# Optimization experiments

Hardware: AMD Instinct MI355X
Metric: run time of the kernel (lower is better)

Reference implementation:

```python
import jax, jax.numpy as jnp
import numpy as np

B, NPG, DEG = 256, 256, 8        # graphs, nodes/graph, avg degree
IN_C, HID, OUT_C = 64, 64, 64
N = B * NPG                      # 65536 nodes
E = N * DEG                      # 524288 edges
K = NPG // 2                     # ASAP ratio=0.5 -> 128 kept nodes per graph


def setup_inputs() -> dict:
    key = jax.random.key(0)
    ks = jax.random.split(key, 12)
    x = jax.random.normal(ks[0], (N, IN_C), jnp.float32)
    # within-graph random edges, no self loops (ASAP adds remaining self loops itself)
    g = jnp.arange(E) // (NPG * DEG)
    src_l = jax.random.randint(ks[1], (E,), 0, NPG)
    off = jax.random.randint(ks[2], (E,), 1, NPG)
    dst_l = (src_l + off) % NPG
    edge_index = jnp.stack([src_l + g * NPG, dst_l + g * NPG]).astype(jnp.int32)
    batch = (jnp.arange(N) // NPG).astype(jnp.int32)
    def lin(k, fi, fo):
        return jax.random.normal(k, (fi, fo), jnp.float32) / np.sqrt(fi)
    return {
        "x": x, "edge_index": edge_index, "batch": batch,
        "W1": lin(ks[3], IN_C, HID), "b1": jnp.zeros((HID,), jnp.float32),
        "lin_W": lin(ks[4], HID, HID), "lin_b": jnp.zeros((HID,), jnp.float32),
        "att_W": lin(ks[5], 2 * HID, 1), "att_b": jnp.zeros((1,), jnp.float32),
        "le1_W": lin(ks[6], HID, 1), "le1_b": jnp.zeros((1,), jnp.float32),
        "le2_W": lin(ks[7], HID, 1),
        "le3_W": lin(ks[8], HID, 1), "le3_b": jnp.zeros((1,), jnp.float32),
        "W2": lin(ks[9], HID, OUT_C), "b2": jnp.zeros((OUT_C,), jnp.float32),
    }


def reference(x, edge_index, batch, W1, b1, lin_W, lin_b, att_W, att_b,
              le1_W, le1_b, le2_W, le3_W, le3_b, W2, b2):
    src, dst = edge_index[0], edge_index[1]
    dt = x.dtype

    # ---- conv1: GCNConv(in, hid) with self loops + symmetric norm ----
    h = x @ W1
    deg = jnp.zeros((N,), dt).at[dst].add(1.0) + 1.0  # +1 self loop
    dinv = jax.lax.rsqrt(deg)
    coef = dinv[src] * dinv[dst]
    h1 = jax.ops.segment_sum(h[src] * coef[:, None], dst, N) \
         + h * (dinv * dinv)[:, None] + b1
    h1 = jax.nn.relu(h1)  # dropout is identity at inference

    # ---- ASAPooling(hid, ratio=0.5): add remaining self loops ----
    sl = jnp.arange(N)
    srcF = jnp.concatenate([src, sl])
    dstF = jnp.concatenate([dst, sl])

    x_pool_j = h1[srcF]                                   # [Ef, HID]
    x_q = jax.ops.segment_max(x_pool_j, dstF, N)          # master-node max
    x_q = (x_q @ lin_W + lin_b)[dstF]
    s = (jnp.concatenate([x_q, x_pool_j], axis=-1) @ att_W + att_b)[:, 0]
    s = jax.nn.leaky_relu(s, 0.2)
    # segment softmax over edges grouped by target
    smax = jax.ops.segment_max(s, dstF, N)
    e = jnp.exp(s - smax[dstF])
    score = e / (jax.ops.segment_sum(e, dstF, N) + 1e-16)[dstF]
    xnew = jax.ops.segment_sum(h1[srcF] * score[:, None], dstF, N)

    # fitness = sigmoid(LEConv(xnew, edges_with_self_loops))
    # LEConv: out_i = sum_{j->i}(lin1(x_j) - lin2(x_i)) + lin3(x_i)
    a = xnew @ le1_W + le1_b
    b2_ = xnew @ le2_W
    degF = jnp.zeros((N,), dt).at[dstF].add(1.0)
    fit = jax.ops.segment_sum(a[srcF], dstF, N)[:, 0] - degF * b2_[:, 0] \
          + (xnew @ le3_W + le3_b)[:, 0]
    fitness = jax.nn.sigmoid(fit)

    # top-k (ratio=0.5) per graph; equal contiguous graphs -> static shapes
    _, topi = jax.lax.top_k(fitness.reshape(B, NPG), K)   # [B, K]
    perm = (topi + jnp.arange(B)[:, None] * NPG).reshape(-1)
    x_sel = xnew[perm] * fitness[perm][:, None]           # [B*K, HID]

    # graph coarsening: A' = S^T A S (dense per graph), diag removed
    g_e = dstF // NPG
    sL = srcF - g_e * NPG
    dL = dstF - g_e * NPG
    A = jnp.zeros((B, NPG, NPG), dt).at[g_e, sL, dL].add(1.0)
    S = jnp.zeros((B, NPG, NPG), dt).at[g_e, sL, dL].add(score)
    Ssel = jnp.take_along_axis(S, topi[:, None, :], axis=2)   # [B, NPG, K]
    AS = jnp.einsum('bij,bjk->bik', A, Ssel)                  # A @ S
    A2 = jnp.einsum('bji,bjk->bik', Ssel, AS)                 # S^T (A S) -> [B,K,K]
    A2 = A2 * (1.0 - jnp.eye(K, dtype=dt))                    # remove_diag

    # ---- conv2: GCNConv(hid, out); returned edge_weight is discarded in
    # the original forward, so edges are binary (nnz of A') + self loops ----
    M = (A2 > 0).astype(dt) + jnp.eye(K, dtype=dt)            # [B, src, dst]
    h2 = (x_sel @ W2).reshape(B, K, OUT_C)
    deg2 = M.sum(axis=1)                                      # in-degree per target
    d2 = jax.lax.rsqrt(deg2)
    Mn = M * d2[:, :, None] * d2[:, None, :]
    out2 = jnp.einsum('bsd,bsf->bdf', Mn, h2) + b2            # [B, K, OUT_C]

    # ---- global_mean_pool over each graph's K kept nodes ----
    return out2.mean(axis=1)                                  # [B, OUT_C]
```

## Files before the change

kernel.cpp:

```cpp
#include <hip/hip_runtime.h>

typedef float f4 __attribute__((ext_vector_type(4)));
typedef unsigned long long u64;

#define NPGL 256
#define EPGL 2048
#define HIDD 64
#define KKEEP 128
#define NTH 1024

__device__ __forceinline__ int swz(int n, int c) {
  return (n << 6) + ((((c ^ n) ^ (n >> 4)) & 15) << 2);
}

__global__ void __launch_bounds__(NTH)
asap_fused(const float* __restrict__ x, const int* __restrict__ ei,
           const float* __restrict__ W1, const float* __restrict__ b1,
           const float* __restrict__ linW, const float* __restrict__ linb,
           const float* __restrict__ attW, const float* __restrict__ attb,
           const float* __restrict__ le1W, const float* __restrict__ le1b,
           const float* __restrict__ le2W,
           const float* __restrict__ le3W, const float* __restrict__ le3b,
           const float* __restrict__ W2, const float* __restrict__ b2,
           float* __restrict__ out, int Etot)
{
  const int g = blockIdx.x;
  const int tid = threadIdx.x;

  __shared__ __align__(16) float buf[NPGL * HIDD];
  __shared__ __align__(16) float mskf[4096];
  __shared__ __align__(16) float esc[EPGL];
  __shared__ __align__(8) unsigned char csrc[4096];
  __shared__ unsigned short rowstU[NPGL + 1];
  __shared__ unsigned short rowstP[NPGL + 1];
  __shared__ int cnt[NPGL];
  __shared__ float dinv_[NPGL];
  __shared__ float sA[NPGL], sB[NPGL];
  __shared__ float rsf[NPGL];
  __shared__ float u_[HIDD], wsum[HIDD];
  __shared__ int scanw[4], scanwP[4];
  __shared__ float c0s;

  u64* Imask = (u64*)mskf;
  u64* Rmask = ((u64*)mskf) + 1024;
  u64* conn  = ((u64*)mskf) + 1536;
  int*   kept = (int*)(mskf + 3584);
  float* d2A  = mskf + 3712;
  float* cA   = mskf + 3840;

  const int ebase = g * EPGL;
  const int nbase = g * NPGL;

  ((u64*)mskf)[tid] = 0ull;
  if (tid < NPGL) { cnt[tid] = 0; ((u64*)mskf)[1536 + tid] = 0ull; }
  __syncthreads();

  int es[2], ed[2];
#pragma unroll
  for (int i = 0; i < 2; ++i) {
    const int e = tid + i * NTH;
    es[i] = ei[ebase + e] - nbase;
    ed[i] = ei[Etot + ebase + e] - nbase;
    atomicAdd(&cnt[ed[i]], 1);
  }
  {
    const f4* xg = (const f4*)(x + (size_t)nbase * HIDD);
#pragma unroll
    for (int ii = 0; ii < 4; ++ii) {
      const int i = tid + ii * NTH;
      *(f4*)&buf[swz(i >> 4, i & 15)] = xg[i];
    }
  }
  __syncthreads();

  int sU = 0, sP = 0, mU = 0;
  if (tid < NPGL) {
    mU = cnt[tid];
    const int mP = (mU + 7) & ~7;
    sU = mU; sP = mP;
#pragma unroll
    for (int off = 1; off < 64; off <<= 1) {
      const int uU = __shfl_up(sU, off, 64);
      const int uP = __shfl_up(sP, off, 64);
      if ((tid & 63) >= off) { sU += uU; sP += uP; }
    }
    if ((tid & 63) == 63) { scanw[tid >> 6] = sU; scanwP[tid >> 6] = sP; }
  }
  __syncthreads();
  if (tid < NPGL) {
    int aU = 0, aP = 0;
    const int w = tid >> 6;
    for (int ww = 0; ww < w; ++ww) { aU += scanw[ww]; aP += scanwP[ww]; }
    rowstU[tid + 1] = (unsigned short)(sU + aU);
    rowstP[tid + 1] = (unsigned short)(sP + aP);
    if (tid == 0) { rowstU[0] = 0; rowstP[0] = 0; }
    cnt[tid] = 0;
    dinv_[tid] = rsqrtf((float)mU + 1.0f);
  }
  if (tid < HIDD) {
    float a = 0.f;
    for (int f = 0; f < HIDD; ++f) a += linW[tid * HIDD + f] * attW[f];
    u_[tid] = a;
  }
  if (tid == 0) {
    float a = 0.f;
    for (int f = 0; f < HIDD; ++f) a += linb[f] * attW[f];
    c0s = a + attb[0];
  }
  __syncthreads();

#pragma unroll
  for (int i = 0; i < 2; ++i) {
    const int j = atomicAdd(&cnt[ed[i]], 1);
    csrc[(int)rowstP[ed[i]] + j] = (unsigned char)es[i];
  }
  if (tid < NPGL) atomicOr(&Imask[tid * 4 + (tid >> 6)], 1ull << (tid & 63));
#pragma unroll
  for (int i = 0; i < 2; ++i)
    atomicOr(&Imask[ed[i] * 4 + (es[i] >> 6)], 1ull << (es[i] & 63));
  __syncthreads();

  {
    const int wv = tid >> 6;
    const int r  = ((wv & 3) << 6) + (tid & 63);
    const int fc = __builtin_amdgcn_readfirstlane(wv >> 2);
    const float* __restrict__ Wg = W1 + fc * 16;
    f4 acc[4];
#pragma unroll
    for (int c = 0; c < 4; ++c) acc[c] = f4{0.f, 0.f, 0.f, 0.f};
#pragma unroll
    for (int p = 0; p < 4; ++p) {
      f4 xa[4];
#pragma unroll
      for (int c = 0; c < 4; ++c) xa[c] = *(const f4*)&buf[swz(r, p * 4 + c)];
#pragma unroll
      for (int kk = 0; kk < 16; ++kk) {
        const int k = p * 16 + kk;
        const float xv = ((const float*)xa)[kk];
        const float* __restrict__ Wk = Wg + k * HIDD;
#pragma unroll
        for (int c = 0; c < 4; ++c)
          acc[c] += xv * *(const f4*)(Wk + c * 4);
      }
    }
    __syncthreads();
#pragma unroll
    for (int c = 0; c < 4; ++c) *(f4*)&buf[swz(r, fc * 4 + c)] = acc[c];
  }
  __syncthreads();

  {
    const int d = tid >> 2, hh = tid & 3;
    const float dd = dinv_[d];
    const int deg = cnt[d];
    const int p0 = rowstP[d];
    f4 acc[4];
#pragma unroll
    for (int j = 0; j < 4; ++j) {
      const int c = hh + 4 * j;
      acc[j] = *(const f4*)&buf[swz(d, c)] * (dd * dd) + *(const f4*)&b1[4 * c];
    }
    const int nb = deg >> 3;
    int j8 = 0;
    for (int b = 0; b < nb; ++b, j8 += 8) {
      const u64 bits = *(const u64*)(csrc + p0 + j8);
#pragma unroll
      for (int t = 0; t < 8; ++t) {
        const int s = (int)((bits >> (8 * t)) & 255);
        const float cf = dinv_[s] * dd;
#pragma unroll
        for (int j = 0; j < 4; ++j)
          acc[j] += cf * *(const f4*)&buf[swz(s, hh + 4 * j)];
      }
    }
    const int rem = deg & 7;
    if (rem) {
      const u64 bits = *(const u64*)(csrc + p0 + j8);
      for (int t = 0; t < rem; ++t) {
        const int s = (int)((bits >> (8 * t)) & 255);
        const float cf = dinv_[s] * dd;
#pragma unroll
        for (int j = 0; j < 4; ++j)
          acc[j] += cf * *(const f4*)&buf[swz(s, hh + 4 * j)];
      }
    }
    float sBp = 0.f;
#pragma unroll
    for (int j = 0; j < 4; ++j) {
      acc[j] = __builtin_elementwise_max(acc[j], f4{0.f, 0.f, 0.f, 0.f});
      const f4 aw = *(const f4*)&attW[HIDD + 4 * (hh + 4 * j)];
      sBp += acc[j].x * aw.x + acc[j].y * aw.y + acc[j].z * aw.z + acc[j].w * aw.w;
    }
    sBp += __shfl_xor(sBp, 1); sBp += __shfl_xor(sBp, 2);
    if (hh == 0) sB[d] = sBp;
    __syncthreads();
#pragma unroll
    for (int j = 0; j < 4; ++j) *(f4*)&buf[swz(d, hh + 4 * j)] = acc[j];
  }
  __syncthreads();

  {
    const int d = tid >> 2, hh = tid & 3;
    const int deg = cnt[d];
    const int p0 = rowstP[d];
    const int q0 = rowstU[d];
    f4 own[4], mx[4];
#pragma unroll
    for (int j = 0; j < 4; ++j) {
      own[j] = *(const f4*)&buf[swz(d, hh + 4 * j)];
      mx[j] = own[j];
    }
    const int nb = deg >> 3;
    int j8 = 0;
    for (int b = 0; b < nb; ++b, j8 += 8) {
      const u64 bits = *(const u64*)(csrc + p0 + j8);
#pragma unroll
      for (int t = 0; t < 8; ++t) {
        const int s = (int)((bits >> (8 * t)) & 255);
#pragma unroll
        for (int j = 0; j < 4; ++j)
          mx[j] = __builtin_elementwise_max(mx[j], *(const f4*)&buf[swz(s, hh + 4 * j)]);
      }
    }
    const int rem = deg & 7;
    if (rem) {
      const u64 bits = *(const u64*)(csrc + p0 + j8);
      for (int t = 0; t < rem; ++t) {
        const int s = (int)((bits >> (8 * t)) & 255);
#pragma unroll
        for (int j = 0; j < 4; ++j)
          mx[j] = __builtin_elementwise_max(mx[j], *(const f4*)&buf[swz(s, hh + 4 * j)]);
      }
    }
    float sAv = 0.f;
#pragma unroll
    for (int j = 0; j < 4; ++j) {
      const f4 uu = *(const f4*)&u_[4 * (hh + 4 * j)];
      sAv += mx[j].x * uu.x + mx[j].y * uu.y + mx[j].z * uu.z + mx[j].w * uu.w;
    }
    sAv += __shfl_xor(sAv, 1); sAv += __shfl_xor(sAv, 2);
    const float sa = c0s + sAv;
    float scS = sa + sB[d];
    scS = scS >= 0.f ? scS : 0.2f * scS;
    float mxv = scS;
#pragma unroll 4
    for (int t = hh; t < deg; t += 4) {
      float sc = sa + sB[csrc[p0 + t]];
      sc = sc >= 0.f ? sc : 0.2f * sc;
      mxv = fmaxf(mxv, sc);
    }
    mxv = fmaxf(mxv, __shfl_xor(mxv, 1));
    mxv = fmaxf(mxv, __shfl_xor(mxv, 2));
    float sum = 0.f;
#pragma unroll 4
    for (int t = hh; t < deg; t += 4) {
      float sc = sa + sB[csrc[p0 + t]];
      sc = sc >= 0.f ? sc : 0.2f * sc;
      const float e = __expf(sc - mxv);
      esc[q0 + t] = e;
      sum += e;
    }
    sum += __shfl_xor(sum, 1); sum += __shfl_xor(sum, 2);
    const float esf = __expf(scS - mxv);
    const float rs = 1.0f / (esf + sum + 1e-16f);
    asm volatile("s_waitcnt lgkmcnt(0)" ::: "memory");
    f4 a[4];
#pragma unroll
    for (int j = 0; j < 4; ++j) a[j] = esf * own[j];
    j8 = 0;
    for (int b = 0; b < nb; ++b, j8 += 8) {
      const u64 bits = *(const u64*)(csrc + p0 + j8);
#pragma unroll
      for (int t = 0; t < 8; ++t) {
        const int s = (int)((bits >> (8 * t)) & 255);
        const float e = esc[q0 + j8 + t];
#pragma unroll
        for (int j = 0; j < 4; ++j)
          a[j] += e * *(const f4*)&buf[swz(s, hh + 4 * j)];
      }
    }
    if (rem) {
      const u64 bits = *(const u64*)(csrc + p0 + j8);
      for (int t = 0; t < rem; ++t) {
        const int s = (int)((bits >> (8 * t)) & 255);
        const float e = esc[q0 + j8 + t];
#pragma unroll
        for (int j = 0; j < 4; ++j)
          a[j] += e * *(const f4*)&buf[swz(s, hh + 4 * j)];
      }
    }
#pragma unroll
    for (int j = 0; j < 4; ++j) a[j] *= rs;
    __syncthreads();
#pragma unroll
    for (int j = 0; j < 4; ++j) *(f4*)&buf[swz(d, hh + 4 * j)] = a[j];
  }
  __syncthreads();

  {
    const int n = tid >> 2, q = tid & 3;
    float av = 0.f, bv = 0.f, cv = 0.f;
#pragma unroll
    for (int j = 0; j < 4; ++j) {
      const int c = q + 4 * j;
      const f4 v = *(const f4*)&buf[swz(n, c)];
      const int k = c * 4;
      av += v.x * le1W[k] + v.y * le1W[k + 1] + v.z * le1W[k + 2] + v.w * le1W[k + 3];
      bv += v.x * le2W[k] + v.y * le2W[k + 1] + v.z * le2W[k + 2] + v.w * le2W[k + 3];
      cv += v.x * le3W[k] + v.y * le3W[k + 1] + v.z * le3W[k + 2] + v.w * le3W[k + 3];
    }
    av += __shfl_xor(av, 1); av += __shfl_xor(av, 2);
    bv += __shfl_xor(bv, 1); bv += __shfl_xor(bv, 2);
    cv += __shfl_xor(cv, 1); cv += __shfl_xor(cv, 2);
    if (q == 0) {
      sA[n] = av + le1b[0];
      sB[n] = bv;
      dinv_[n] = cv + le3b[0];
    }
  }
  __syncthreads();
  {
    const int d = tid >> 2, q = tid & 3;
    const int deg = cnt[d];
    const int p0 = rowstP[d];
    float fp = 0.f;
#pragma unroll 4
    for (int t = q; t < deg; t += 4) fp += sA[csrc[p0 + t]];
    fp += __shfl_xor(fp, 1); fp += __shfl_xor(fp, 2);
    if (q == 0) {
      float f = sA[d] + fp;
      f -= (float)(deg + 1) * sB[d];
      f += dinv_[d];
      float sg;
      if (f >= 0.f) sg = 1.f / (1.f + expf(-f));
      else { const float t2 = expf(f); sg = t2 / (1.f + t2); }
      rsf[d] = sg;
    }
  }
  __syncthreads();

  {
    const int n = tid >> 2, q = tid & 3;
    const float fn = rsf[n];
    int r = 0;
    for (int m = q * 64; m < q * 64 + 64; ++m) {
      const float fm = rsf[m];
      r += ((fm > fn) || (fm == fn && m < n)) ? 1 : 0;
    }
    r += __shfl_xor(r, 1); r += __shfl_xor(r, 2);
    if (q == 0 && r < KKEEP) kept[r] = n;
  }
  __syncthreads();

  if (tid < KKEEP * 4) {
    const int q = tid >> 2, w = tid & 3;
    const int kq = kept[q];
    u64 acc = 0ull;
#pragma unroll
    for (int ww = 0; ww < 4; ++ww) {
      u64 bits = Imask[kq * 4 + ww];
      while (bits) {
        const int m = (ww << 6) + __builtin_ctzll(bits);
        bits &= bits - 1;
        acc |= Imask[m * 4 + w];
      }
    }
    Rmask[q * 4 + w] = acc;
  }
  __syncthreads();
  if (tid < KKEEP * 4) {
    const int p = tid >> 2, wb = tid & 3;
    const int kp = kept[p];
    const u64 I0 = Imask[kp * 4 + 0], I1 = Imask[kp * 4 + 1],
              I2 = Imask[kp * 4 + 2], I3 = Imask[kp * 4 + 3];
    u64 bits = 0ull;
    for (int j = 0; j < 32; ++j) {
      const int q = wb * 32 + j;
      if (q == p) continue;
      const u64* R = &Rmask[q * 4];
      if ((I0 & R[0]) | (I1 & R[1]) | (I2 & R[2]) | (I3 & R[3]))
        bits |= 1ull << (q & 63);
    }
    atomicOr(&conn[p * 2 + (wb >> 1)], bits);
  }
  __syncthreads();

  if (tid < KKEEP * 4) {
    const int q = tid >> 2, h = tid & 3;
    const int w = q >> 6, sh = q & 63;
    int c = 0;
    for (int p = h * 32; p < h * 32 + 32; ++p)
      c += (int)((conn[p * 2 + w] >> sh) & 1ull);
    c += __shfl_xor(c, 1); c += __shfl_xor(c, 2);
    if (h == 0) d2A[q] = rsqrtf((float)(c + 1));
  }
  __syncthreads();
  if (tid < KKEEP * 4) {
    const int s = tid >> 2, h = tid & 3;
    unsigned int b32 = (unsigned int)(conn[s * 2 + (h >> 1)] >> (32 * (h & 1)));
    const int base = ((h >> 1) << 6) + ((h & 1) << 5);
    float acc = 0.f;
    while (b32) {
      const int d_ = base + __builtin_ctz(b32);
      b32 &= b32 - 1;
      acc += d2A[d_];
    }
    acc += __shfl_xor(acc, 1); acc += __shfl_xor(acc, 2);
    if (h == 0)
      cA[s] = d2A[s] * (d2A[s] + acc) * rsf[kept[s]] * (1.0f / (float)KKEEP);
  }
  __syncthreads();

  {
    const int f = tid & 63, blk = tid >> 6;
    float p = 0.f;
    for (int j = 0; j < 8; ++j) {
      const int s = blk * 8 + j;
      const int ks = kept[s];
      const int off = (ks << 6) + (((((f >> 2) ^ ks) ^ (ks >> 4)) & 15) << 2) + (f & 3);
      p += cA[s] * buf[off];
    }
    esc[blk * 64 + f] = p;
  }
  __syncthreads();
  if (tid < HIDD) {
    float s = 0.f;
#pragma unroll
    for (int b = 0; b < 16; ++b) s += esc[b * 64 + tid];
    wsum[tid] = s;
  }
  __syncthreads();
  if (tid < HIDD) {
    float o = b2[tid];
    for (int k = 0; k < HIDD; ++k) o += wsum[k] * W2[k * HIDD + tid];
    out[(size_t)g * HIDD + tid] = o;
  }
}

extern "C" void kernel_launch(void* const* d_in, const int* in_sizes, int n_in,
                              void* d_out, int out_size, void* d_ws, size_t ws_size,
                              hipStream_t stream) {
  (void)n_in; (void)out_size; (void)d_ws; (void)ws_size;
  const float* x    = (const float*)d_in[0];
  const int*   ei   = (const int*)d_in[1];
  const float* W1   = (const float*)d_in[3];
  const float* b1   = (const float*)d_in[4];
  const float* linW = (const float*)d_in[5];
  const float* linb = (const float*)d_in[6];
  const float* attW = (const float*)d_in[7];
  const float* attb = (const float*)d_in[8];
  const float* le1W = (const float*)d_in[9];
  const float* le1b = (const float*)d_in[10];
  const float* le2W = (const float*)d_in[11];
  const float* le3W = (const float*)d_in[12];
  const float* le3b = (const float*)d_in[13];
  const float* W2   = (const float*)d_in[14];
  const float* b2   = (const float*)d_in[15];
  const int Etot = in_sizes[1] / 2;
  const int nGraphs = 256;

  asap_fused<<<dim3(nGraphs), dim3(NTH), 0, stream>>>(
      x, ei, W1, b1, linW, linb, attW, attb, le1W, le1b, le2W, le3W, le3b,
      W2, b2, (float*)d_out, Etot);
}
```

Baseline: 58.24 us.

## Use padded LDS rows, prescale by dinv, split accumulators in edge gathers

The XOR-swizzled node-feature layout in shared memory is replaced by plain rows padded to a stride of 72 floats, which simplifies the gather address math. The GCN normalisation is folded into the transform epilogue: rows are pre-multiplied by dinv, so the per-edge multiply and the dinv lookup disappear. The sum, max and weighted-sum gather loops now alternate between two accumulator sets to shorten dependency chains. The softmax max is taken over raw sB values before a single leaky-ReLU, which is valid because leaky-ReLU is monotone. The trade-off is a larger shared-memory footprint and possibly different LDS bank-conflict behaviour.

Result: faster. 51.31 us (-11.9%).

```diff
diff --git a/kernel.cpp b/kernel.cpp
--- a/kernel.cpp
+++ b/kernel.cpp
@@ -8,10 +8,9 @@
 #define HIDD 64
 #define KKEEP 128
 #define NTH 1024
-
-__device__ __forceinline__ int swz(int n, int c) {
-  return (n << 6) + ((((c ^ n) ^ (n >> 4)) & 15) << 2);
-}
+#define RSTR 72
+
+__device__ __forceinline__ int ro(int n, int c) { return n * RSTR + c * 4; }
 
 __global__ void __launch_bounds__(NTH)
 asap_fused(const float* __restrict__ x, const int* __restrict__ ei,
@@ -27,7 +26,7 @@
   const int g = blockIdx.x;
   const int tid = threadIdx.x;
 
-  __shared__ __align__(16) float buf[NPGL * HIDD];
+  __shared__ __align__(16) float buf[NPGL * RSTR];
   __shared__ __align__(16) float mskf[4096];
   __shared__ __align__(16) float esc[EPGL];
   __shared__ __align__(8) unsigned char csrc[4096];
@@ -68,7 +67,7 @@
 #pragma unroll
     for (int ii = 0; ii < 4; ++ii) {
       const int i = tid + ii * NTH;
-      *(f4*)&buf[swz(i >> 4, i & 15)] = xg[i];
+      *(f4*)&buf[ro(i >> 4, i & 15)] = xg[i];
     }
   }
   __syncthreads();
@@ -132,7 +131,7 @@
     for (int p = 0; p < 4; ++p) {
       f4 xa[4];
 #pragma unroll
-      for (int c = 0; c < 4; ++c) xa[c] = *(const f4*)&buf[swz(r, p * 4 + c)];
+      for (int c = 0; c < 4; ++c) xa[c] = *(const f4*)&buf[ro(r, p * 4 + c)];
 #pragma unroll
       for (int kk = 0; kk < 16; ++kk) {
         const int k = p * 16 + kk;
@@ -143,9 +142,10 @@
           acc[c] += xv * *(const f4*)(Wk + c * 4);
       }
     }
+    const float dv = dinv_[r];
     __syncthreads();
 #pragma unroll
-    for (int c = 0; c < 4; ++c) *(f4*)&buf[swz(r, fc * 4 + c)] = acc[c];
+    for (int c = 0; c < 4; ++c) *(f4*)&buf[ro(r, fc * 4 + c)] = acc[c] * dv;
   }
   __syncthreads();
 
@@ -154,11 +154,12 @@
     const float dd = dinv_[d];
     const int deg = cnt[d];
     const int p0 = rowstP[d];
-    f4 acc[4];
+    const int hb = ro(0, hh);
+    f4 acc[4], acc2[4];
 #pragma unroll
     for (int j = 0; j < 4; ++j) {
-      const int c = hh + 4 * j;
-      acc[j] = *(const f4*)&buf[swz(d, c)] * (dd * dd) + *(const f4*)&b1[4 * c];
+      acc[j] = *(const f4*)&buf[ro(d, hh) + j * 16];
+      acc2[j] = f4{0.f, 0.f, 0.f, 0.f};
     }
     const int nb = deg >> 3;
     int j8 = 0;
@@ -167,10 +168,14 @@
 #pragma unroll
       for (int t = 0; t < 8; ++t) {
         const int s = (int)((bits >> (8 * t)) & 255);
-        const float cf = dinv_[s] * dd;
-#pragma unroll
-        for (int j = 0; j < 4; ++j)
-          acc[j] += cf * *(const f4*)&buf[swz(s, hh + 4 * j)];
+        const int base = s * RSTR + hb;
+        if (t & 1) {
+#pragma unroll
+          for (int j = 0; j < 4; ++j) acc2[j] += *(const f4*)&buf[base + j * 16];
+        } else {
+#pragma unroll
+          for (int j = 0; j < 4; ++j) acc[j] += *(const f4*)&buf[base + j * 16];
+        }
       }
     }
     const int rem = deg & 7;
@@ -178,15 +183,15 @@
       const u64 bits = *(const u64*)(csrc + p0 + j8);
       for (int t = 0; t < rem; ++t) {
         const int s = (int)((bits >> (8 * t)) & 255);
-        const float cf = dinv_[s] * dd;
-#pragma unroll
-        for (int j = 0; j < 4; ++j)
-          acc[j] += cf * *(const f4*)&buf[swz(s, hh + 4 * j)];
+        const int base = s * RSTR + hb;
+#pragma unroll
+        for (int j = 0; j < 4; ++j) acc[j] += *(const f4*)&buf[base + j * 16];
       }
     }
     float sBp = 0.f;
 #pragma unroll
     for (int j = 0; j < 4; ++j) {
+      acc[j] = (acc[j] + acc2[j]) * dd + *(const f4*)&b1[4 * (hh + 4 * j)];
       acc[j] = __builtin_elementwise_max(acc[j], f4{0.f, 0.f, 0.f, 0.f});
       const f4 aw = *(const f4*)&attW[HIDD + 4 * (hh + 4 * j)];
       sBp += acc[j].x * aw.x + acc[j].y * aw.y + acc[j].z * aw.z + acc[j].w * aw.w;
@@ -195,7 +200,7 @@
     if (hh == 0) sB[d] = sBp;
     __syncthreads();
 #pragma unroll
-    for (int j = 0; j < 4; ++j) *(f4*)&buf[swz(d, hh + 4 * j)] = acc[j];
+    for (int j = 0; j < 4; ++j) *(f4*)&buf[ro(d, hh) + j * 16] = acc[j];
   }
   __syncthreads();
 
@@ -204,11 +209,13 @@
     const int deg = cnt[d];
     const int p0 = rowstP[d];
     const int q0 = rowstU[d];
-    f4 own[4], mx[4];
+    const int hb = hh * 4;
+    f4 own[4], mx[4], mx2[4];
 #pragma unroll
     for (int j = 0; j < 4; ++j) {
-      own[j] = *(const f4*)&buf[swz(d, hh + 4 * j)];
+      own[j] = *(const f4*)&buf[ro(d, hh) + j * 16];
       mx[j] = own[j];
+      mx2[j] = own[j];
     }
     const int nb = deg >> 3;
     int j8 = 0;
@@ -217,9 +224,16 @@
 #pragma unroll
       for (int t = 0; t < 8; ++t) {
         const int s = (int)((bits >> (8 * t)) & 255);
-#pragma unroll
-        for (int j = 0; j < 4; ++j)
-          mx[j] = __builtin_elementwise_max(mx[j], *(const f4*)&buf[swz(s, hh + 4 * j)]);
+        const int base = s * RSTR + hb;
+        if (t & 1) {
+#pragma unroll
+          for (int j = 0; j < 4; ++j)
+            mx2[j] = __builtin_elementwise_max(mx2[j], *(const f4*)&buf[base + j * 16]);
+        } else {
+#pragma unroll
+          for (int j = 0; j < 4; ++j)
+            mx[j] = __builtin_elementwise_max(mx[j], *(const f4*)&buf[base + j * 16]);
+        }
       }
     }
     const int rem = deg & 7;
@@ -227,30 +241,29 @@
       const u64 bits = *(const u64*)(csrc + p0 + j8);
       for (int t = 0; t < rem; ++t) {
         const int s = (int)((bits >> (8 * t)) & 255);
+        const int base = s * RSTR + hb;
 #pragma unroll
         for (int j = 0; j < 4; ++j)
-          mx[j] = __builtin_elementwise_max(mx[j], *(const f4*)&buf[swz(s, hh + 4 * j)]);
+          mx[j] = __builtin_elementwise_max(mx[j], *(const f4*)&buf[base + j * 16]);
       }
     }
     float sAv = 0.f;
 #pragma unroll
     for (int j = 0; j < 4; ++j) {
+      mx[j] = __builtin_elementwise_max(mx[j], mx2[j]);
       const f4 uu = *(const f4*)&u_[4 * (hh + 4 * j)];
       sAv += mx[j].x * uu.x + mx[j].y * uu.y + mx[j].z * uu.z + mx[j].w * uu.w;
     }
     sAv += __shfl_xor(sAv, 1); sAv += __shfl_xor(sAv, 2);
     const float sa = c0s + sAv;
-    float scS = sa + sB[d];
-    scS = scS >= 0.f ? scS : 0.2f * scS;
-    float mxv = scS;
+    const float sBd = sB[d];
+    float mxB = sBd;
 #pragma unroll 4
-    for (int t = hh; t < deg; t += 4) {
-      float sc = sa + sB[csrc[p0 + t]];
-      sc = sc >= 0.f ? sc : 0.2f * sc;
-      mxv = fmaxf(mxv, sc);
-    }
-    mxv = fmaxf(mxv, __shfl_xor(mxv, 1));
-    mxv = fmaxf(mxv, __shfl_xor(mxv, 2));
+    for (int t = hh; t < deg; t += 4) mxB = fmaxf(mxB, sB[csrc[p0 + t]]);
+    mxB = fmaxf(mxB, __shfl_xor(mxB, 1));
+    mxB = fmaxf(mxB, __shfl_xor(mxB, 2));
+    float mxv = sa + mxB;
+    mxv = mxv >= 0.f ? mxv : 0.2f * mxv;
     float sum = 0.f;
 #pragma unroll 4
     for (int t = hh; t < deg; t += 4) {
@@ -261,12 +274,14 @@
       sum += e;
     }
     sum += __shfl_xor(sum, 1); sum += __shfl_xor(sum, 2);
+    float scS = sa + sBd;
+    scS = scS >= 0.f ? scS : 0.2f * scS;
     const float esf = __expf(scS - mxv);
     const float rs = 1.0f / (esf + sum + 1e-16f);
     asm volatile("s_waitcnt lgkmcnt(0)" ::: "memory");
-    f4 a[4];
-#pragma unroll
-    for (int j = 0; j < 4; ++j) a[j] = esf * own[j];
+    f4 a[4], a2[4];
+#pragma unroll
+    for (int j = 0; j < 4; ++j) { a[j] = esf * own[j]; a2[j] = f4{0.f, 0.f, 0.f, 0.f}; }
     j8 = 0;
     for (int b = 0; b < nb; ++b, j8 += 8) {
       const u64 bits = *(const u64*)(csrc + p0 + j8);
@@ -274,9 +289,14 @@
       for (int t = 0; t < 8; ++t) {
         const int s = (int)((bits >> (8 * t)) & 255);
         const float e = esc[q0 + j8 + t];
-#pragma unroll
-        for (int j = 0; j < 4; ++j)
-          a[j] += e * *(const f4*)&buf[swz(s, hh + 4 * j)];
+        const int base = s * RSTR + hb;
+        if (t & 1) {
+#pragma unroll
+          for (int j = 0; j < 4; ++j) a2[j] += e * *(const f4*)&buf[base + j * 16];
+        } else {
+#pragma unroll
+          for (int j = 0; j < 4; ++j) a[j] += e * *(const f4*)&buf[base + j * 16];
+        }
       }
     }
     if (rem) {
@@ -284,16 +304,16 @@
       for (int t = 0; t < rem; ++t) {
         const int s = (int)((bits >> (8 * t)) & 255);
         const float e = esc[q0 + j8 + t];
-#pragma unroll
-        for (int j = 0; j < 4; ++j)
-          a[j] += e * *(const f4*)&buf[swz(s, hh + 4 * j)];
-      }
-    }
-#pragma unroll
-    for (int j = 0; j < 4; ++j) a[j] *= rs;
+        const int base = s * RSTR + hb;
+#pragma unroll
+        for (int j = 0; j < 4; ++j) a[j] += e * *(const f4*)&buf[base + j * 16];
+      }
+    }
+#pragma unroll
+    for (int j = 0; j < 4; ++j) a[j] = (a[j] + a2[j]) * rs;
     __syncthreads();
 #pragma unroll
-    for (int j = 0; j < 4; ++j) *(f4*)&buf[swz(d, hh + 4 * j)] = a[j];
+    for (int j = 0; j < 4; ++j) *(f4*)&buf[ro(d, hh) + j * 16] = a[j];
   }
   __syncthreads();
 
@@ -303,7 +323,7 @@
 #pragma unroll
     for (int j = 0; j < 4; ++j) {
       const int c = q + 4 * j;
-      const f4 v = *(const f4*)&buf[swz(n, c)];
+      const f4 v = *(const f4*)&buf[ro(n, q) + j * 16];
       const int k = c * 4;
       av += v.x * le1W[k] + v.y * le1W[k + 1] + v.z * le1W[k + 2] + v.w * le1W[k + 3];
       bv += v.x * le2W[k] + v.y * le2W[k + 1] + v.z * le2W[k + 2] + v.w * le2W[k + 3];
@@ -417,8 +437,7 @@
     for (int j = 0; j < 8; ++j) {
       const int s = blk * 8 + j;
       const int ks = kept[s];
-      const int off = (ks << 6) + (((((f >> 2) ^ ks) ^ (ks >> 4)) & 15) << 2) + (f & 3);
-      p += cA[s] * buf[off];
+      p += cA[s] * buf[ks * RSTR + f];
     }
     esc[blk * 64 + f] = p;
   }
```
